# Kernel tuning notes

Measured on AMD Instinct MI355X. Metric: run time of the kernel, lower is better.

## Reference

```python
import jax, jax.numpy as jnp
import numpy as np

LOSS_WEIGHT = 1.0


def setup_inputs() -> dict:
    key = jax.random.key(0)
    k1, k2 = jax.random.split(key)
    source = jax.random.normal(k1, (8, 4096, 3), dtype=jnp.float32)
    target = jax.random.normal(k2, (8, 4096, 3), dtype=jnp.float32)
    return {"source": source, "target": target}


def reference(source, target):
    # Pairwise Euclidean distances via the Gram-matrix identity (same math as torch.cdist):
    # d(i,j)^2 = ||s_i||^2 + ||t_j||^2 - 2 <s_i, t_j>
    s2 = jnp.sum(source * source, axis=-1)  # [B, N]
    t2 = jnp.sum(target * target, axis=-1)  # [B, M]
    cross = jnp.einsum("bnd,bmd->bnm", source, target)  # [B, N, M]
    d2 = s2[:, :, None] + t2[:, None, :] - 2.0 * cross
    dists = jnp.sqrt(jnp.maximum(d2, 0.0))  # [B, N, M]
    term1 = jnp.mean(jnp.min(dists, axis=2), axis=1)  # source -> nearest target
    term2 = jnp.mean(jnp.min(dists, axis=1), axis=1)  # target -> nearest source
    return LOSS_WEIGHT * (jnp.mean(term1) + jnp.mean(term2))
```

## Files before the change

### kernel.cpp

```cpp
#include <hip/hip_runtime.h>

#define BB 8
#define NN 4096
#define BLK 512
#define RPT 8
#define ROWS 128
#define SLICES 32
#define JSL (NN/SLICES)
#define PADJ (JSL + 1)
#define NWAVE (BLK/64)
#define MAGIC 0x3A9C6E17u

__device__ __forceinline__ float min3f(float a, float b, float c) {
    float d;
    asm("v_min3_f32 %0, %1, %2, %3" : "=v"(d) : "v"(a), "v"(b), "v"(c));
    return d;
}

__global__ __launch_bounds__(BLK, 4) void cd_main(const float* __restrict__ src,
                                                  const float* __restrict__ tgt,
                                                  unsigned long long* __restrict__ flag,
                                                  float* __restrict__ out) {
    __shared__ float4 tl[SLICES * PADJ];
    __shared__ float pmin[NWAVE * ROWS];
    __shared__ float bsum[NWAVE];
    const int dir = blockIdx.z;
    const float* Sp = dir ? tgt : src;
    const float* Tp = dir ? src : tgt;
    const int b   = blockIdx.y;
    const int rt  = blockIdx.x;
    const int tid = threadIdx.x;

    const float* tb = Tp + (size_t)b * NN * 3;
    for (int g = tid; g < NN/4; g += BLK) {
        const float4* t4 = (const float4*)(tb + 12*g);
        float4 v0 = t4[0], v1 = t4[1], v2 = t4[2];
        float px[4] = {v0.x, v0.w, v1.z, v2.y};
        float py[4] = {v0.y, v1.x, v1.w, v2.z};
        float pz[4] = {v0.z, v1.y, v2.x, v2.w};
        int k0 = 4*g;
        int base = (k0 >> 7) * PADJ + (k0 & (JSL - 1));
#pragma unroll
        for (int i = 0; i < 4; ++i)
            tl[base + i] = make_float4(px[i], py[i], pz[i],
                                       0.5f*(px[i]*px[i] + py[i]*py[i] + pz[i]*pz[i]));
    }

    const float* sb = Sp + (size_t)b * NN * 3;
    const int sub   = tid & 15;
    const int slice = tid >> 4;
    const int rowBase = rt * ROWS;
    float nx[RPT], ny[RPT], nz[RPT], q[RPT];
#pragma unroll
    for (int r = 0; r < RPT; ++r) {
        int row = rowBase + sub + 16*r;
        float x = sb[3*row], y = sb[3*row+1], z = sb[3*row+2];
        nx[r] = -x; ny[r] = -y; nz[r] = -z;
        q[r] = 0.5f*(x*x + y*y + z*z);
    }
    __syncthreads();

    float m[RPT];
#pragma unroll
    for (int r = 0; r < RPT; ++r) m[r] = 1.0e30f;

    const float4* tp = tl + slice * PADJ;
#pragma unroll 2
    for (int j = 0; j < JSL; j += 2) {
        float4 t0 = tp[j];
        float4 t1 = tp[j+1];
#pragma unroll
        for (int r = 0; r < RPT; ++r) {
            float a0 = fmaf(nx[r], t0.x, fmaf(ny[r], t0.y, fmaf(nz[r], t0.z, t0.w)));
            float a1 = fmaf(nx[r], t1.x, fmaf(ny[r], t1.y, fmaf(nz[r], t1.z, t1.w)));
            m[r] = min3f(m[r], a0, a1);
        }
    }

#pragma unroll
    for (int r = 0; r < RPT; ++r) {
        float v = m[r];
        v = fminf(v, __shfl_xor(v, 16, 64));
        v = fminf(v, __shfl_xor(v, 32, 64));
        m[r] = v + q[r];
    }
    const int wid = tid >> 6;
    if ((tid & 63) < 16) {
#pragma unroll
        for (int r = 0; r < RPT; ++r)
            pmin[wid*ROWS + sub + 16*r] = m[r];
    }
    __syncthreads();

    float dsum = 0.0f;
    if (tid < ROWS) {
        float v = pmin[tid];
#pragma unroll
        for (int s = 1; s < NWAVE; ++s) v = fminf(v, pmin[s*ROWS + tid]);
        v = fmaxf(v, 0.0f);
        dsum = sqrtf(2.0f * v);
    }
#pragma unroll
    for (int o = 32; o > 0; o >>= 1) dsum += __shfl_down(dsum, o, 64);
    if ((tid & 63) == 0) bsum[tid >> 6] = dsum;
    __syncthreads();
    if (tid == 0) {
        float t = 0.0f;
#pragma unroll
        for (int w = 0; w < NWAVE; ++w) t += bsum[w];
        const int idx = ((dir * BB + b) * 32) + rt;
        unsigned long long pk = ((unsigned long long)MAGIC << 32)
                              | (unsigned long long)__float_as_uint(t);
        __hip_atomic_store(&flag[idx], pk, __ATOMIC_RELAXED, __HIP_MEMORY_SCOPE_AGENT);
    }

    if ((rt | b | dir) == 0) {
        __syncthreads();
        unsigned long long v;
        do {
            __builtin_amdgcn_s_sleep(1);
            v = __hip_atomic_load(&flag[tid], __ATOMIC_RELAXED, __HIP_MEMORY_SCOPE_AGENT);
        } while ((unsigned)(v >> 32) != MAGIC);
        float val = __uint_as_float((unsigned)(v & 0xFFFFFFFFull));
#pragma unroll
        for (int o = 32; o > 0; o >>= 1) val += __shfl_down(val, o, 64);
        if ((tid & 63) == 0) bsum[tid >> 6] = val;
        __syncthreads();
        if (tid == 0) {
            float t = 0.0f;
#pragma unroll
            for (int w = 0; w < NWAVE; ++w) t += bsum[w];
            out[0] = t * (1.0f / (float)(BB * NN));
        }
    }
}

extern "C" void kernel_launch(void* const* d_in, const int* in_sizes, int n_in,
                              void* d_out, int out_size, void* d_ws, size_t ws_size,
                              hipStream_t stream) {
    const float* src = (const float*)d_in[0];
    const float* tgt = (const float*)d_in[1];
    unsigned long long* flag = (unsigned long long*)d_ws;
    float* out = (float*)d_out;

    dim3 grid(NN/ROWS, BB, 2);
    cd_main<<<grid, BLK, 0, stream>>>(src, tgt, flag, out);
}
```

Measured before the change: 76.78 us.

## Stage target points in two LDS halves to raise occupancy

After: 75.89 us. No clear change (-1.2%).

```diff
diff --git a/kernel.cpp b/kernel.cpp
--- a/kernel.cpp
+++ b/kernel.cpp
@@ -6,8 +6,9 @@
 #define RPT 8
 #define ROWS 128
 #define SLICES 32
-#define JSL (NN/SLICES)
-#define PADJ (JSL + 1)
+#define HALF 2048
+#define JSLH (HALF/SLICES)
+#define PADH (JSLH + 1)
 #define NWAVE (BLK/64)
 #define MAGIC 0x3A9C6E17u
 
@@ -17,11 +18,11 @@
     return d;
 }
 
-__global__ __launch_bounds__(BLK, 4) void cd_main(const float* __restrict__ src,
+__global__ __launch_bounds__(BLK, 8) void cd_main(const float* __restrict__ src,
                                                   const float* __restrict__ tgt,
                                                   unsigned long long* __restrict__ flag,
                                                   float* __restrict__ out) {
-    __shared__ float4 tl[SLICES * PADJ];
+    __shared__ float4 tl[SLICES * PADH];
     __shared__ float pmin[NWAVE * ROWS];
     __shared__ float bsum[NWAVE];
     const int dir = blockIdx.z;
@@ -32,19 +33,6 @@
     const int tid = threadIdx.x;
 
     const float* tb = Tp + (size_t)b * NN * 3;
-    for (int g = tid; g < NN/4; g += BLK) {
-        const float4* t4 = (const float4*)(tb + 12*g);
-        float4 v0 = t4[0], v1 = t4[1], v2 = t4[2];
-        float px[4] = {v0.x, v0.w, v1.z, v2.y};
-        float py[4] = {v0.y, v1.x, v1.w, v2.z};
-        float pz[4] = {v0.z, v1.y, v2.x, v2.w};
-        int k0 = 4*g;
-        int base = (k0 >> 7) * PADJ + (k0 & (JSL - 1));
-#pragma unroll
-        for (int i = 0; i < 4; ++i)
-            tl[base + i] = make_float4(px[i], py[i], pz[i],
-                                       0.5f*(px[i]*px[i] + py[i]*py[i] + pz[i]*pz[i]));
-    }
 
     const float* sb = Sp + (size_t)b * NN * 3;
     const int sub   = tid & 15;
@@ -58,22 +46,34 @@
         nx[r] = -x; ny[r] = -y; nz[r] = -z;
         q[r] = 0.5f*(x*x + y*y + z*z);
     }
-    __syncthreads();
 
     float m[RPT];
 #pragma unroll
     for (int r = 0; r < RPT; ++r) m[r] = 1.0e30f;
 
-    const float4* tp = tl + slice * PADJ;
+    for (int h = 0; h < 2; ++h) {
+        if (h) __syncthreads();
+#pragma unroll
+        for (int i = 0; i < HALF/BLK; ++i) {
+            int k = tid + i*BLK;
+            const float* p = tb + (size_t)h*(HALF*3) + 3*k;
+            float x = p[0], y = p[1], z = p[2];
+            tl[(k >> 6) * PADH + (k & (JSLH - 1))] =
+                make_float4(x, y, z, 0.5f*(x*x + y*y + z*z));
+        }
+        __syncthreads();
+
+        const float4* tp = tl + slice * PADH;
 #pragma unroll 2
-    for (int j = 0; j < JSL; j += 2) {
-        float4 t0 = tp[j];
-        float4 t1 = tp[j+1];
+        for (int j = 0; j < JSLH; j += 2) {
+            float4 t0 = tp[j];
+            float4 t1 = tp[j+1];
 #pragma unroll
-        for (int r = 0; r < RPT; ++r) {
-            float a0 = fmaf(nx[r], t0.x, fmaf(ny[r], t0.y, fmaf(nz[r], t0.z, t0.w)));
-            float a1 = fmaf(nx[r], t1.x, fmaf(ny[r], t1.y, fmaf(nz[r], t1.z, t1.w)));
-            m[r] = min3f(m[r], a0, a1);
+            for (int r = 0; r < RPT; ++r) {
+                float a0 = fmaf(nx[r], t0.x, fmaf(ny[r], t0.y, fmaf(nz[r], t0.z, t0.w)));
+                float a1 = fmaf(nx[r], t1.x, fmaf(ny[r], t1.y, fmaf(nz[r], t1.z, t1.w)));
+                m[r] = min3f(m[r], a0, a1);
+            }
         }
     }
 
@@ -85,6 +85,7 @@
         m[r] = v + q[r];
     }
     const int wid = tid >> 6;
+    __syncthreads();
     if ((tid & 63) < 16) {
 #pragma unroll
         for (int r = 0; r < RPT; ++r)
```
